# Kernel tuning notes

Hardware: AMD Instinct MI355X
Metric: run time of the kernel (lower is better)

Reference implementation:

```python
import jax, jax.numpy as jnp
import numpy as np

B, N, C, H, P, DP = 2, 1024, 768, 12, 4, 64
CH = C // H
SCALE = CH ** -0.5
EPS = 1e-5


def setup_inputs() -> dict:
    key = jax.random.key(0)
    ks = jax.random.split(key, 24)
    w = lambda k, s: jax.random.normal(k, s, jnp.float32) * 0.02
    inp = {
        'single': jax.random.normal(ks[0], (B, N, C), jnp.float32),
        'pair': jax.random.normal(ks[1], (B, N, N, DP), jnp.float32),
        'rot': jax.random.normal(ks[2], (B, N, 3, 3), jnp.float32),
        'trans': jax.random.normal(ks[3], (B, N, 3), jnp.float32),
        'mask': jnp.ones((B, N), dtype=bool),
        'Wq': w(ks[4], (C, C)), 'bq': jnp.zeros((C,), jnp.float32),
        'Wk': w(ks[5], (C, C)), 'bk': jnp.zeros((C,), jnp.float32),
        'Wv': w(ks[6], (C, C)), 'bv': jnp.zeros((C,), jnp.float32),
        'Wpb': w(ks[7], (DP, H)), 'bpb': jnp.zeros((H,), jnp.float32),
        'Wqp': w(ks[8], (C, H * P * 3)), 'bqp': jnp.zeros((H * P * 3,), jnp.float32),
        'Wkp': w(ks[9], (C, H * P * 3)), 'bkp': jnp.zeros((H * P * 3,), jnp.float32),
        'Wvp': w(ks[10], (C, H * P * 3)), 'bvp': jnp.zeros((H * P * 3,), jnp.float32),
        'Wo': w(ks[11], (C, C)), 'bo': jnp.zeros((C,), jnp.float32),
        'Wpo': w(ks[12], (H * P * 3, C)), 'bpo': jnp.zeros((C,), jnp.float32),
        'gamma': jnp.ones((C,), jnp.float32), 'beta': jnp.zeros((C,), jnp.float32),
    }
    return inp


def _ipa(single, pair, rot, trans, mask,
         Wq, bq, Wk, bk, Wv, bv, Wpb, bpb,
         Wqp, bqp, Wkp, bkp, Wvp, bvp,
         Wo, bo, Wpo, bpo, gamma, beta):
    # scalar q/k/v: [B,N,H,CH]
    q = (single @ Wq + bq).reshape(B, N, H, CH)
    k = (single @ Wk + bk).reshape(B, N, H, CH)
    v = (single @ Wv + bv).reshape(B, N, H, CH)
    # pair bias: [B,H,N,N]
    pair_bias = jnp.transpose(pair @ Wpb + bpb, (0, 3, 1, 2))
    # point q/k/v in local frames: [B,N,H,P,3]
    q_pts = (single @ Wqp + bqp).reshape(B, N, H, P, 3)
    k_pts = (single @ Wkp + bkp).reshape(B, N, H, P, 3)
    v_pts = (single @ Wvp + bvp).reshape(B, N, H, P, 3)
    # rotate into global frame and translate
    t = trans[:, :, None, None, :]  # [B,N,1,1,3]
    rt = lambda pts: jnp.einsum('bnhpd,bnde->bnhpe', pts, rot) + t
    q_pts, k_pts, v_pts = rt(q_pts), rt(k_pts), rt(v_pts)
    # squared norms: [B,H,N]
    q2 = jnp.transpose((q_pts ** 2).sum((3, 4)), (0, 2, 1))
    k2 = jnp.transpose((k_pts ** 2).sum((3, 4)), (0, 2, 1))
    # logits [B,H,M,N]
    scalar_logits = jnp.einsum('bmhc,bnhc->bhmn', q, k) * SCALE
    qk_pts = jnp.einsum('bmhpd,bnhpd->bhmn', q_pts, k_pts)
    point_logits = -0.5 * (q2[:, :, :, None] + k2[:, :, None, :] - 2.0 * qk_pts) * SCALE
    logits = scalar_logits + point_logits + pair_bias
    mask2d = mask[:, None, :, None] & mask[:, None, None, :]
    logits = jnp.where(mask2d, logits, -1e9)
    attn = jax.nn.softmax(logits, axis=-1)
    # dual output aggregation
    out_scalar = jnp.einsum('bhmn,bnhc->bmhc', attn, v).reshape(B, N, C)
    out_points = jnp.einsum('bhmn,bnhpd->bmhpd', attn, v_pts).reshape(B, N, H * P * 3)
    out = (out_scalar @ Wo + bo) + (out_points @ Wpo + bpo)
    x = single + out
    mu = x.mean(-1, keepdims=True)
    var = ((x - mu) ** 2).mean(-1, keepdims=True)
    return (x - mu) * jax.lax.rsqrt(var + EPS) * gamma + beta


def reference(single, pair, rot, trans, mask,
              Wq, bq, Wk, bk, Wv, bv, Wpb, bpb,
              Wqp, bqp, Wkp, bkp, Wvp, bvp,
              Wo, bo, Wpo, bpo, gamma, beta):
    return _ipa(single, pair, rot, trans, mask,
                Wq, bq, Wk, bk, Wv, bv, Wpb, bpb,
                Wqp, bqp, Wkp, bkp, Wvp, bvp,
                Wo, bo, Wpo, bpo, gamma, beta)
```

## Files before the change

kernel.cpp:

```cpp
#include <hip/hip_runtime.h>
#include <hip/hip_bf16.h>

#define B_ 2
#define N_ 1024
#define C_ 768
#define H_ 12
#define CH_ 64
#define P_ 4
#define DP_ 64
#define HP3 144
#define SCALE_ 0.125f
#define FATS 2816
#define K2_ 960
#define NCHUNK 2

typedef __attribute__((ext_vector_type(8))) short short8;
typedef __attribute__((ext_vector_type(4))) float f32x4;

__device__ __forceinline__ short f2bf(float f) {
  __hip_bfloat16 h = __float2bfloat16(f);
  return *reinterpret_cast<short*>(&h);
}
__device__ __forceinline__ float bf2f(unsigned short u) {
  __hip_bfloat16 h;
  *reinterpret_cast<unsigned short*>(&h) = u;
  return __bfloat162float(h);
}

__global__ __launch_bounds__(256) void prep_misc(
    const float* __restrict__ single, unsigned short* __restrict__ Sbf,
    const float* __restrict__ Wq, const float* __restrict__ Wk,
    const float* __restrict__ Wv, const float* __restrict__ Wqp,
    const float* __restrict__ Wkp, const float* __restrict__ Wvp,
    unsigned short* __restrict__ WT1,
    const float* __restrict__ Wo, const float* __restrict__ Wpo,
    unsigned short* __restrict__ W2T,
    const float* __restrict__ bq, const float* __restrict__ bk,
    const float* __restrict__ bv, const float* __restrict__ bqp,
    const float* __restrict__ bkp, const float* __restrict__ bvp,
    const float* __restrict__ bo, const float* __restrict__ bpo,
    float* __restrict__ bcat1, float* __restrict__ bias2)
{
  __shared__ float t[16][17];
  const int tid = threadIdx.x;
  const int bid = blockIdx.x;
  if (bid < 8448) {
    const int bx = bid % 48, by = bid / 48;
    const int rr = tid >> 4, cc = tid & 15;
    const int kk0 = bx * 16, nn0 = by * 16;
    const float* W = nullptr; int ncol0 = 0, Nw = 768;
    if (nn0 < 2304) {
      int s = nn0 / 768;
      W = (s == 0) ? Wq : (s == 1 ? Wk : Wv);
      ncol0 = nn0 - s * 768; Nw = 768;
    } else if (nn0 < 2736) {
      int s = (nn0 - 2304) / 144;
      W = (s == 0) ? Wqp : (s == 1 ? Wkp : Wvp);
      ncol0 = nn0 - 2304 - s * 144; Nw = 144;
    }
    t[rr][cc] = W ? W[(size_t)(kk0 + rr) * Nw + ncol0 + cc] : 0.f;
    __syncthreads();
    WT1[(size_t)(nn0 + rr) * 768 + kk0 + cc] = (unsigned short)f2bf(t[cc][rr]);
  } else if (bid < 11328) {
    const int lb = bid - 8448;
    const int bx = lb % 60, by = lb / 60;
    const int rr = tid >> 4, cc = tid & 15;
    const int kk0 = bx * 16, nn0 = by * 16;
    const int k2 = kk0 + rr, h = k2 / 80, c80 = k2 - h * 80;
    float v = 0.f;
    if (c80 < 64)      v = Wo[(size_t)(h * 64 + c80) * 768 + nn0 + cc];
    else if (c80 < 76) v = Wpo[(size_t)(h * 12 + c80 - 64) * 768 + nn0 + cc];
    t[rr][cc] = v;
    __syncthreads();
    W2T[(size_t)(nn0 + rr) * 960 + kk0 + cc] = (unsigned short)f2bf(t[cc][rr]);
  } else if (bid < 11339) {
    const int idx = (bid - 11328) * 256 + tid;
    if (idx < 2816) {
      float v = 0.f;
      if (idx < 2304) { int s = idx / 768; const float* p = s == 0 ? bq : (s == 1 ? bk : bv); v = p[idx - s * 768]; }
      else if (idx < 2736) { int s = (idx - 2304) / 144; const float* p = s == 0 ? bqp : (s == 1 ? bkp : bvp); v = p[idx - 2304 - s * 144]; }
      bcat1[idx] = v;
    }
    if (idx < 768) bias2[idx] = bo[idx] + bpo[idx];
  } else {
    const int idx = (bid - 11339) * 256 + tid;
    const float4 v = reinterpret_cast<const float4*>(single)[idx];
    union { unsigned short u[4]; uint2 v2; } o;
    o.u[0] = (unsigned short)f2bf(v.x); o.u[1] = (unsigned short)f2bf(v.y);
    o.u[2] = (unsigned short)f2bf(v.z); o.u[3] = (unsigned short)f2bf(v.w);
    reinterpret_cast<uint2*>(Sbf)[idx] = o.v2;
  }
}

template<int BM>
__global__ __launch_bounds__(256) void gemm_bf16(
    const unsigned short* __restrict__ A, int lda,
    const unsigned short* __restrict__ BT, int ldb, int K,
    float* __restrict__ out, int ldo, const float* __restrict__ bias)
{
  constexpr int BN = 64;
  constexpr int MI = BM / 32;
  constexpr int NJ = 2;
  __shared__ __align__(16) unsigned short As[BM][40];
  __shared__ __align__(16) unsigned short Bs[BN][40];
  const int tid = threadIdx.x;
  const int w = tid >> 6, l = tid & 63, r16 = l & 15, g = l >> 4;
  const int wr = w >> 1, wc = w & 1;
  const int bm = blockIdx.y * BM, bn = blockIdx.x * BN;
  f32x4 acc[MI][NJ];
  #pragma unroll
  for (int mi = 0; mi < MI; ++mi)
    #pragma unroll
    for (int nj = 0; nj < NJ; ++nj) {
      acc[mi][nj][0] = 0.f; acc[mi][nj][1] = 0.f;
      acc[mi][nj][2] = 0.f; acc[mi][nj][3] = 0.f;
    }
  for (int k0 = 0; k0 < K; k0 += 32) {
    #pragma unroll
    for (int i = 0; i < BM / 64; ++i) {
      const int idx = tid + 256 * i;
      const int row = idx >> 2, q4 = idx & 3;
      *(uint4*)&As[row][q4 * 8] =
          *(const uint4*)&A[(size_t)(bm + row) * lda + k0 + q4 * 8];
    }
    {
      const int row = tid >> 2, q4 = tid & 3;
      if (row < BN)
        *(uint4*)&Bs[row][q4 * 8] =
            *(const uint4*)&BT[(size_t)(bn + row) * ldb + k0 + q4 * 8];
    }
    __syncthreads();
    short8 af[MI], bfr[NJ];
    #pragma unroll
    for (int mi = 0; mi < MI; ++mi)
      af[mi] = *(const short8*)&As[wr * (BM / 2) + mi * 16 + r16][g * 8];
    #pragma unroll
    for (int nj = 0; nj < NJ; ++nj)
      bfr[nj] = *(const short8*)&Bs[wc * 32 + nj * 16 + r16][g * 8];
    #pragma unroll
    for (int mi = 0; mi < MI; ++mi)
      #pragma unroll
      for (int nj = 0; nj < NJ; ++nj)
        acc[mi][nj] = __builtin_amdgcn_mfma_f32_16x16x32_bf16(
            af[mi], bfr[nj], acc[mi][nj], 0, 0, 0);
    __syncthreads();
  }
  #pragma unroll
  for (int mi = 0; mi < MI; ++mi)
    #pragma unroll
    for (int nj = 0; nj < NJ; ++nj) {
      const int n = bn + wc * 32 + nj * 16 + r16;
      const float bn_ = bias[n];
      #pragma unroll
      for (int reg = 0; reg < 4; ++reg) {
        const int m = bm + wr * (BM / 2) + mi * 16 + g * 4 + reg;
        out[(size_t)m * ldo + n] = acc[mi][nj][reg] + bn_;
      }
    }
}

__global__ __launch_bounds__(128) void prep_qkv(
    const float* __restrict__ fat, const float* __restrict__ rot,
    const float* __restrict__ trans,
    __hip_bfloat16* __restrict__ Qaug, __hip_bfloat16* __restrict__ Kaug,
    __hip_bfloat16* __restrict__ Vtg)
{
  __shared__ float pts[3][12];
  __shared__ float s2[2];
  const int tid = threadIdx.x;
  const int bn = blockIdx.x, h = blockIdx.y;
  const int b = bn >> 10, n = bn & 1023;
  const int bh = b * H_ + h;
  const float* row = fat + (size_t)bn * FATS;
  if (tid < 36) {
    const int set = tid / 12, j = tid - set * 12;
    const int p = j / 3, e = j - p * 3;
    const float* src = row + 2304 + set * 144 + h * 12 + p * 3;
    const float d0 = src[0], d1 = src[1], d2 = src[2];
    const float* rr = rot + (size_t)bn * 9;
    pts[set][j] = d0 * rr[e] + d1 * rr[3 + e] + d2 * rr[6 + e]
                  + trans[(size_t)bn * 3 + e];
  }
  __syncthreads();
  if (tid < 2) {
    float s = 0.f;
    #pragma unroll
    for (int j = 0; j < 12; ++j) s += pts[tid][j] * pts[tid][j];
    s2[tid] = s;
  }
  __syncthreads();
  const int c = tid;
  if (c < 96) {
    float qv, kv;
    if (c < 64) {
      qv = SCALE_ * row[h * CH_ + c];
      kv = row[768 + h * CH_ + c];
    } else if (c < 76) {
      qv = SCALE_ * pts[0][c - 64];
      kv = pts[1][c - 64];
    } else if (c == 76) {
      qv = -0.5f * SCALE_ * s2[0];
      kv = 1.0f;
    } else if (c == 77) {
      qv = -0.5f * SCALE_;
      kv = s2[1];
    } else { qv = 0.f; kv = 0.f; }
    const size_t orow = ((size_t)bh << 10) + n;
    Qaug[orow * 96 + c] = __float2bfloat16(qv);
    Kaug[orow * 96 + c] = __float2bfloat16(kv);
  }
  if (c < 80) {
    float vv = 0.f;
    if (c < 64) vv = row[1536 + h * CH_ + c];
    else if (c < 76) vv = pts[2][c - 64];
    Vtg[(((size_t)bh * 80 + c) << 10) + n] = __float2bfloat16(vv);
  }
}

__global__ __launch_bounds__(256) void pair_bias_mfma(
    const float* __restrict__ pair, const float* __restrict__ Wpb,
    const float* __restrict__ bpb, unsigned short* __restrict__ pb)
{
  __shared__ __align__(16) short WpbT[16][72];
  __shared__ float bpb_s[16];
  __shared__ unsigned short PBs[256][18];
  const int tid = threadIdx.x;
  const int w = tid >> 6, l = tid & 63, r16 = l & 15, g = l >> 4;
  const size_t F0 = (size_t)blockIdx.x * 256;
  const int b = (int)(F0 >> 20);
  const int mn0 = (int)(F0 & 1048575);
  #pragma unroll
  for (int i = 0; i < 4; ++i) {
    int idx = tid + 256 * i;
    int hh = idx & 15, d = idx >> 4;
    WpbT[hh][d] = f2bf(hh < 12 ? Wpb[d * 12 + hh] : 0.f);
  }
  if (tid < 16) bpb_s[tid] = (tid < 12) ? bpb[tid] : 0.f;
  __syncthreads();
  const float4* p4 = (const float4*)pair;
  #pragma unroll
  for (int rg = 0; rg < 4; ++rg) {
    const size_t Fr = F0 + w * 64 + rg * 16 + r16;
    const float bias = bpb_s[r16];
    f32x4 acc;
    acc[0] = bias; acc[1] = bias; acc[2] = bias; acc[3] = bias;
    #pragma unroll
    for (int ks = 0; ks < 2; ++ks) {
      const float4 a0 = p4[Fr * 16 + g * 2 + ks * 8];
      const float4 a1 = p4[Fr * 16 + g * 2 + ks * 8 + 1];
      short8 ap;
      ap[0] = f2bf(a0.x); ap[1] = f2bf(a0.y); ap[2] = f2bf(a0.z); ap[3] = f2bf(a0.w);
      ap[4] = f2bf(a1.x); ap[5] = f2bf(a1.y); ap[6] = f2bf(a1.z); ap[7] = f2bf(a1.w);
      const short8 bw = *(const short8*)&WpbT[r16][ks * 32 + g * 8];
      acc = __builtin_amdgcn_mfma_f32_16x16x32_bf16(ap, bw, acc, 0, 0, 0);
    }
    #pragma unroll
    for (int reg = 0; reg < 4; ++reg)
      PBs[w * 64 + rg * 16 + 4 * g + reg][r16] = (unsigned short)f2bf(acc[reg]);
  }
  __syncthreads();
  #pragma unroll
  for (int hh = 0; hh < 12; ++hh)
    pb[((size_t)(b * 12 + hh) << 20) + mn0 + tid] = PBs[tid][hh];
}

__global__ __launch_bounds__(256) void flash_attn_part(
    const __hip_bfloat16* __restrict__ Qaug, const __hip_bfloat16* __restrict__ Kaug,
    const __hip_bfloat16* __restrict__ Vtg, const unsigned short* __restrict__ pb,
    float* __restrict__ pacc, float* __restrict__ pml)
{
  __shared__ __align__(16) short Ks[64][104];
  __shared__ __align__(16) short Vt[80][72];
  __shared__ __align__(16) short Ps[64][72];
  const int tid = threadIdx.x;
  const int w = tid >> 6, l = tid & 63, r16 = l & 15, g = l >> 4;
  const int m0 = blockIdx.x * 64;
  const int h = blockIdx.y;
  const int b = blockIdx.z >> 1, chunk = blockIdx.z & 1;
  const int bh = b * H_ + h;
  const uint4* Kg = (const uint4*)Kaug;
  const uint4* Vg = (const uint4*)Vtg;
  short8 qreg[3];
  {
    const unsigned short* qrow =
        (const unsigned short*)Qaug + (size_t)((bh << 10) + m0 + w * 16 + r16) * 96;
    #pragma unroll
    for (int ks = 0; ks < 3; ++ks)
      qreg[ks] = *(const short8*)&qrow[ks * 32 + g * 8];
  }
  float rm[4], rl[4];
  f32x4 acc[5];
  #pragma unroll
  for (int r = 0; r < 4; ++r) { rm[r] = -1e30f; rl[r] = 0.f; }
  #pragma unroll
  for (int ct = 0; ct < 5; ++ct) {
    acc[ct][0] = 0.f; acc[ct][1] = 0.f; acc[ct][2] = 0.f; acc[ct][3] = 0.f;
  }
  for (int t = chunk * (16 / NCHUNK); t < (chunk + 1) * (16 / NCHUNK); ++t) {
    const int n0 = t * 64;
    {
      const int r = tid >> 2, q = tid & 3;
      #pragma unroll
      for (int i = 0; i < 3; ++i) {
        const int c8 = q + 4 * i;
        *(uint4*)&Ks[r][c8 * 8] = Kg[(size_t)((bh << 10) + n0 + r) * 12 + c8];
      }
      #pragma unroll
      for (int i = 0; i < 3; ++i) {
        const int ch = tid + 256 * i;
        if (ch < 640) {
          const int cc = ch >> 3, j8 = ch & 7;
          *(uint4*)&Vt[cc][j8 * 8] = Vg[(size_t)(bh * 80 + cc) * 128 + (n0 >> 3) + j8];
        }
      }
    }
    f32x4 s[4];
    {
      const unsigned short* pbrow = pb + ((size_t)bh << 20) + n0 + r16;
      #pragma unroll
      for (int j = 0; j < 4; ++j)
        #pragma unroll
        for (int reg = 0; reg < 4; ++reg)
          s[j][reg] = bf2f(pbrow[((size_t)(m0 + w * 16 + 4 * g + reg) << 10) + 16 * j]);
    }
    __syncthreads();
    #pragma unroll
    for (int ks = 0; ks < 3; ++ks) {
      #pragma unroll
      for (int j = 0; j < 4; ++j) {
        const short8 bK = *(const short8*)&Ks[16 * j + r16][ks * 32 + g * 8];
        s[j] = __builtin_amdgcn_mfma_f32_16x16x32_bf16(qreg[ks], bK, s[j], 0, 0, 0);
      }
    }
    #pragma unroll
    for (int reg = 0; reg < 4; ++reg) {
      float tm = fmaxf(fmaxf(s[0][reg], s[1][reg]), fmaxf(s[2][reg], s[3][reg]));
      tm = fmaxf(tm, __shfl_xor(tm, 1));
      tm = fmaxf(tm, __shfl_xor(tm, 2));
      tm = fmaxf(tm, __shfl_xor(tm, 4));
      tm = fmaxf(tm, __shfl_xor(tm, 8));
      const float nm = fmaxf(rm[reg], tm);
      const float fac = __expf(rm[reg] - nm);
      rm[reg] = nm;
      float ps = 0.f;
      #pragma unroll
      for (int j = 0; j < 4; ++j) {
        const float p = __expf(s[j][reg] - nm);
        s[j][reg] = p;
        ps += p;
      }
      ps += __shfl_xor(ps, 1);
      ps += __shfl_xor(ps, 2);
      ps += __shfl_xor(ps, 4);
      ps += __shfl_xor(ps, 8);
      rl[reg] = rl[reg] * fac + ps;
      #pragma unroll
      for (int ct = 0; ct < 5; ++ct) acc[ct][reg] *= fac;
    }
    #pragma unroll
    for (int j = 0; j < 4; ++j)
      #pragma unroll
      for (int reg = 0; reg < 4; ++reg)
        Ps[w * 16 + 4 * g + reg][16 * j + r16] = f2bf(s[j][reg]);
    __syncthreads();
    #pragma unroll
    for (int ks = 0; ks < 2; ++ks) {
      const short8 aP = *(const short8*)&Ps[w * 16 + r16][ks * 32 + g * 8];
      #pragma unroll
      for (int ct = 0; ct < 5; ++ct) {
        const short8 bV = *(const short8*)&Vt[ct * 16 + r16][ks * 32 + g * 8];
        acc[ct] = __builtin_amdgcn_mfma_f32_16x16x32_bf16(aP, bV, acc[ct], 0, 0, 0);
      }
    }
    __syncthreads();
  }
  #pragma unroll
  for (int reg = 0; reg < 4; ++reg) {
    const int row = (bh << 10) + m0 + w * 16 + 4 * g + reg;
    const size_t base = ((size_t)chunk * 24576 + row) * 80;
    #pragma unroll
    for (int ct = 0; ct < 5; ++ct)
      pacc[base + ct * 16 + r16] = acc[ct][reg];
    if (r16 == 0) {
      pml[((size_t)chunk * 24576 + row) * 2]     = rm[reg];
      pml[((size_t)chunk * 24576 + row) * 2 + 1] = rl[reg];
    }
  }
}

__global__ __launch_bounds__(256) void flash_combine(
    const float* __restrict__ pacc, const float* __restrict__ pml,
    unsigned short* __restrict__ fused)
{
  const int tid = threadIdx.x;
  const int r = tid >> 4, cg = tid & 15;
  const int row = blockIdx.x * 16 + r;
  const int bh = row >> 10, m = row & 1023;
  const int b = bh / 12, h = bh - b * 12;
  const float m0 = pml[(size_t)row * 2], l0 = pml[(size_t)row * 2 + 1];
  const float m1 = pml[((size_t)24576 + row) * 2], l1 = pml[((size_t)24576 + row) * 2 + 1];
  const float M = fmaxf(m0, m1);
  const float w0 = __expf(m0 - M), w1 = __expf(m1 - M);
  const float inv = 1.f / (l0 * w0 + l1 * w1);
  const size_t mg = (size_t)(b * N_ + m);
  #pragma unroll
  for (int i = 0; i < 5; ++i) {
    const int c = cg * 5 + i;
    const float a0 = pacc[(size_t)row * 80 + c];
    const float a1 = pacc[((size_t)24576 + row) * 80 + c];
    fused[mg * K2_ + h * 80 + c] = (unsigned short)f2bf((a0 * w0 + a1 * w1) * inv);
  }
}

__global__ __launch_bounds__(256) void ln_kernel(
    const float* __restrict__ single, const float* __restrict__ tmp,
    const float* __restrict__ gamma, const float* __restrict__ beta,
    float* __restrict__ out)
{
  __shared__ float x_s[C_];
  __shared__ float rs1[4], rs2[4];
  const int row = blockIdx.x, tid = threadIdx.x;
  const int lane = tid & 63, wave = tid >> 6;
  const size_t base = (size_t)row * C_;
  float s1 = 0.f, s2 = 0.f;
  for (int i = tid; i < C_; i += 256) {
    float x = single[base + i] + tmp[base + i];
    x_s[i] = x;
    s1 += x;
    s2 += x * x;
  }
  #pragma unroll
  for (int off = 32; off > 0; off >>= 1) {
    s1 += __shfl_xor(s1, off);
    s2 += __shfl_xor(s2, off);
  }
  if (!lane) { rs1[wave] = s1; rs2[wave] = s2; }
  __syncthreads();
  const float S1 = rs1[0] + rs1[1] + rs1[2] + rs1[3];
  const float S2 = rs2[0] + rs2[1] + rs2[2] + rs2[3];
  const float mu = S1 * (1.f / C_);
  const float var = S2 * (1.f / C_) - mu * mu;
  const float inv = rsqrtf(var + 1e-5f);
  for (int i = tid; i < C_; i += 256)
    out[base + i] = (x_s[i] - mu) * inv * gamma[i] + beta[i];
}

extern "C" void kernel_launch(void* const* d_in, const int* in_sizes, int n_in,
                              void* d_out, int out_size, void* d_ws, size_t ws_size,
                              hipStream_t stream) {
  const float* single = (const float*)d_in[0];
  const float* pair   = (const float*)d_in[1];
  const float* rot    = (const float*)d_in[2];
  const float* trans  = (const float*)d_in[3];
  const float* Wq  = (const float*)d_in[5];
  const float* bq  = (const float*)d_in[6];
  const float* Wk  = (const float*)d_in[7];
  const float* bk  = (const float*)d_in[8];
  const float* Wv  = (const float*)d_in[9];
  const float* bv  = (const float*)d_in[10];
  const float* Wpb = (const float*)d_in[11];
  const float* bpb = (const float*)d_in[12];
  const float* Wqp = (const float*)d_in[13];
  const float* bqp = (const float*)d_in[14];
  const float* Wkp = (const float*)d_in[15];
  const float* bkp = (const float*)d_in[16];
  const float* Wvp = (const float*)d_in[17];
  const float* bvp = (const float*)d_in[18];
  const float* Wo  = (const float*)d_in[19];
  const float* bo  = (const float*)d_in[20];
  const float* Wpo = (const float*)d_in[21];
  const float* bpo = (const float*)d_in[22];
  const float* gamma = (const float*)d_in[23];
  const float* beta  = (const float*)d_in[24];

  float* ws = (float*)d_ws;
  float* fat  = ws;
  float* tmpb = ws + 5767168;
  unsigned short* pbb  = (unsigned short*)(ws + 7340032);
  __hip_bfloat16* Qaug = (__hip_bfloat16*)(ws + 19922944);
  __hip_bfloat16* Kaug = (__hip_bfloat16*)(ws + 21102592);
  __hip_bfloat16* Vtg  = (__hip_bfloat16*)(ws + 22282240);
  unsigned short* Sbf  = (unsigned short*)(ws + 23265280);
  unsigned short* WT1  = (unsigned short*)(ws + 24051712);
  unsigned short* W2T  = (unsigned short*)(ws + 25133056);
  float* bcat1 = ws + 25501696;
  float* bias2 = ws + 25504512;
  unsigned short* fusedb = (unsigned short*)(ws + 25505536);
  float* pacc = ws + 26488576;
  float* pml  = ws + 30420736;

  const dim3 blk(256);
  prep_misc<<<12875, blk, 0, stream>>>(single, Sbf, Wq, Wk, Wv, Wqp, Wkp, Wvp,
                                       WT1, Wo, Wpo, W2T, bq, bk, bv, bqp, bkp,
                                       bvp, bo, bpo, bcat1, bias2);
  gemm_bf16<128><<<dim3(44, 16), blk, 0, stream>>>(Sbf, 768, WT1, 768, 768,
                                                   fat, FATS, bcat1);
  prep_qkv<<<dim3(2048, 12), dim3(128), 0, stream>>>(fat, rot, trans, Qaug, Kaug, Vtg);
  pair_bias_mfma<<<8192, blk, 0, stream>>>(pair, Wpb, bpb, pbb);
  flash_attn_part<<<dim3(16, 12, 2 * NCHUNK), blk, 0, stream>>>(
      Qaug, Kaug, Vtg, pbb, pacc, pml);
  flash_combine<<<1536, blk, 0, stream>>>(pacc, pml, fusedb);
  gemm_bf16<64><<<dim3(12, 32), blk, 0, stream>>>(fusedb, K2_, W2T, K2_, K2_,
                                                  tmpb, 768, bias2);
  ln_kernel<<<2048, blk, 0, stream>>>(single, tmpb, gamma, beta, (float*)d_out);
}
```

Measured before the change: 249.3 us.

## Fuse pair-bias projection into flash attention with 8-way key split

Merges the pair-bias MFMA kernel into the attention kernel, so each block computes the bias tile for all 12 heads in shared memory and consumes it immediately. This removes the bf16 pair-bias round trip through global memory. The key dimension is split into 8 chunks, K and V are read directly from global rather than staged in LDS, and the partial accumulators are stored in bf16. The trade-offs are a larger combine step, extra rounding of the partials, and higher register pressure from three heads per wave.

```diff
diff --git a/kernel.cpp b/kernel.cpp
--- a/kernel.cpp
+++ b/kernel.cpp
@@ -12,7 +12,7 @@
 #define SCALE_ 0.125f
 #define FATS 2816
 #define K2_ 960
-#define NCHUNK 2
+#define NCH 8
 
 typedef __attribute__((ext_vector_type(8))) short short8;
 typedef __attribute__((ext_vector_type(4))) float f32x4;
@@ -217,179 +217,171 @@
   }
 }
 
-__global__ __launch_bounds__(256) void pair_bias_mfma(
+__global__ __launch_bounds__(256) void ipa_fused(
     const float* __restrict__ pair, const float* __restrict__ Wpb,
-    const float* __restrict__ bpb, unsigned short* __restrict__ pb)
+    const float* __restrict__ bpb,
+    const __hip_bfloat16* __restrict__ Qaug,
+    const __hip_bfloat16* __restrict__ Kaug,
+    const __hip_bfloat16* __restrict__ Vtg,
+    unsigned short* __restrict__ pacc, float* __restrict__ pml)
 {
   __shared__ __align__(16) short WpbT[16][72];
   __shared__ float bpb_s[16];
-  __shared__ unsigned short PBs[256][18];
+  __shared__ unsigned short pb_s[12 * 1058];
+  __shared__ __align__(16) unsigned short Ps[4 * 1056];
   const int tid = threadIdx.x;
   const int w = tid >> 6, l = tid & 63, r16 = l & 15, g = l >> 4;
-  const size_t F0 = (size_t)blockIdx.x * 256;
-  const int b = (int)(F0 >> 20);
-  const int mn0 = (int)(F0 & 1048575);
-  #pragma unroll
-  for (int i = 0; i < 4; ++i) {
-    int idx = tid + 256 * i;
-    int hh = idx & 15, d = idx >> 4;
+  const int bid = blockIdx.x;
+  const int combo = bid & 15, mtile = bid >> 4;
+  const int b = combo >> 3, chunk = combo & 7;
+  const int m0 = mtile * 16;
+
+  for (int i = tid; i < 1024; i += 256) {
+    const int hh = i & 15, d = i >> 4;
     WpbT[hh][d] = f2bf(hh < 12 ? Wpb[d * 12 + hh] : 0.f);
   }
   if (tid < 16) bpb_s[tid] = (tid < 12) ? bpb[tid] : 0.f;
+
+  short8 qf[3][3];
+  #pragma unroll
+  for (int hh = 0; hh < 3; ++hh) {
+    const int bh = b * H_ + w * 3 + hh;
+    const unsigned short* qrow = (const unsigned short*)Qaug
+        + (size_t)((bh << 10) + m0 + r16) * 96;
+    #pragma unroll
+    for (int ks = 0; ks < 3; ++ks)
+      qf[hh][ks] = *(const short8*)&qrow[ks * 32 + g * 8];
+  }
+  float rm[3][4], rl[3][4];
+  f32x4 oacc[3][5];
+  #pragma unroll
+  for (int hh = 0; hh < 3; ++hh) {
+    #pragma unroll
+    for (int r = 0; r < 4; ++r) { rm[hh][r] = -1e30f; rl[hh][r] = 0.f; }
+    #pragma unroll
+    for (int ct = 0; ct < 5; ++ct) {
+      oacc[hh][ct][0] = 0.f; oacc[hh][ct][1] = 0.f;
+      oacc[hh][ct][2] = 0.f; oacc[hh][ct][3] = 0.f;
+    }
+  }
   __syncthreads();
-  const float4* p4 = (const float4*)pair;
-  #pragma unroll
-  for (int rg = 0; rg < 4; ++rg) {
-    const size_t Fr = F0 + w * 64 + rg * 16 + r16;
-    const float bias = bpb_s[r16];
-    f32x4 acc;
-    acc[0] = bias; acc[1] = bias; acc[2] = bias; acc[3] = bias;
-    #pragma unroll
-    for (int ks = 0; ks < 2; ++ks) {
-      const float4 a0 = p4[Fr * 16 + g * 2 + ks * 8];
-      const float4 a1 = p4[Fr * 16 + g * 2 + ks * 8 + 1];
-      short8 ap;
-      ap[0] = f2bf(a0.x); ap[1] = f2bf(a0.y); ap[2] = f2bf(a0.z); ap[3] = f2bf(a0.w);
-      ap[4] = f2bf(a1.x); ap[5] = f2bf(a1.y); ap[6] = f2bf(a1.z); ap[7] = f2bf(a1.w);
-      const short8 bw = *(const short8*)&WpbT[r16][ks * 32 + g * 8];
-      acc = __builtin_amdgcn_mfma_f32_16x16x32_bf16(ap, bw, acc, 0, 0, 0);
-    }
-    #pragma unroll
-    for (int reg = 0; reg < 4; ++reg)
-      PBs[w * 64 + rg * 16 + 4 * g + reg][r16] = (unsigned short)f2bf(acc[reg]);
-  }
-  __syncthreads();
-  #pragma unroll
-  for (int hh = 0; hh < 12; ++hh)
-    pb[((size_t)(b * 12 + hh) << 20) + mn0 + tid] = PBs[tid][hh];
-}
-
-__global__ __launch_bounds__(256) void flash_attn_part(
-    const __hip_bfloat16* __restrict__ Qaug, const __hip_bfloat16* __restrict__ Kaug,
-    const __hip_bfloat16* __restrict__ Vtg, const unsigned short* __restrict__ pb,
-    float* __restrict__ pacc, float* __restrict__ pml)
-{
-  __shared__ __align__(16) short Ks[64][104];
-  __shared__ __align__(16) short Vt[80][72];
-  __shared__ __align__(16) short Ps[64][72];
-  const int tid = threadIdx.x;
-  const int w = tid >> 6, l = tid & 63, r16 = l & 15, g = l >> 4;
-  const int m0 = blockIdx.x * 64;
-  const int h = blockIdx.y;
-  const int b = blockIdx.z >> 1, chunk = blockIdx.z & 1;
-  const int bh = b * H_ + h;
-  const uint4* Kg = (const uint4*)Kaug;
-  const uint4* Vg = (const uint4*)Vtg;
-  short8 qreg[3];
-  {
-    const unsigned short* qrow =
-        (const unsigned short*)Qaug + (size_t)((bh << 10) + m0 + w * 16 + r16) * 96;
-    #pragma unroll
-    for (int ks = 0; ks < 3; ++ks)
-      qreg[ks] = *(const short8*)&qrow[ks * 32 + g * 8];
-  }
-  float rm[4], rl[4];
-  f32x4 acc[5];
-  #pragma unroll
-  for (int r = 0; r < 4; ++r) { rm[r] = -1e30f; rl[r] = 0.f; }
-  #pragma unroll
-  for (int ct = 0; ct < 5; ++ct) {
-    acc[ct][0] = 0.f; acc[ct][1] = 0.f; acc[ct][2] = 0.f; acc[ct][3] = 0.f;
-  }
-  for (int t = chunk * (16 / NCHUNK); t < (chunk + 1) * (16 / NCHUNK); ++t) {
-    const int n0 = t * 64;
-    {
-      const int r = tid >> 2, q = tid & 3;
-      #pragma unroll
-      for (int i = 0; i < 3; ++i) {
-        const int c8 = q + 4 * i;
-        *(uint4*)&Ks[r][c8 * 8] = Kg[(size_t)((bh << 10) + n0 + r) * 12 + c8];
-      }
-      #pragma unroll
-      for (int i = 0; i < 3; ++i) {
-        const int ch = tid + 256 * i;
-        if (ch < 640) {
-          const int cc = ch >> 3, j8 = ch & 7;
-          *(uint4*)&Vt[cc][j8 * 8] = Vg[(size_t)(bh * 80 + cc) * 128 + (n0 >> 3) + j8];
+
+  for (int t = 0; t < 2; ++t) {
+    const int n0 = chunk * 128 + t * 64;
+    #pragma unroll 4
+    for (int sub = 0; sub < 16; ++sub) {
+      const int fr = w * 256 + sub * 16 + r16;
+      const int ml = fr >> 6, nn = fr & 63;
+      const float* src = pair
+          + ((((size_t)(b << 10) + m0 + ml) << 10) + n0 + nn) * 64;
+      f32x4 a;
+      a[0] = bpb_s[r16]; a[1] = a[0]; a[2] = a[0]; a[3] = a[0];
+      #pragma unroll
+      for (int ks = 0; ks < 2; ++ks) {
+        const f32x4 a0 = __builtin_nontemporal_load(
+            reinterpret_cast<const f32x4*>(src + ks * 32 + g * 8));
+        const f32x4 a1 = __builtin_nontemporal_load(
+            reinterpret_cast<const f32x4*>(src + ks * 32 + g * 8 + 4));
+        short8 ap;
+        ap[0] = f2bf(a0[0]); ap[1] = f2bf(a0[1]); ap[2] = f2bf(a0[2]); ap[3] = f2bf(a0[3]);
+        ap[4] = f2bf(a1[0]); ap[5] = f2bf(a1[1]); ap[6] = f2bf(a1[2]); ap[7] = f2bf(a1[3]);
+        const short8 bw = *(const short8*)&WpbT[r16][ks * 32 + g * 8];
+        a = __builtin_amdgcn_mfma_f32_16x16x32_bf16(ap, bw, a, 0, 0, 0);
+      }
+      if (r16 < 12) {
+        #pragma unroll
+        for (int reg = 0; reg < 4; ++reg) {
+          const int fr2 = w * 256 + sub * 16 + 4 * g + reg;
+          pb_s[r16 * 1058 + (fr2 >> 6) * 66 + (fr2 & 63)] =
+              (unsigned short)f2bf(a[reg]);
         }
       }
     }
-    f32x4 s[4];
-    {
-      const unsigned short* pbrow = pb + ((size_t)bh << 20) + n0 + r16;
+    __syncthreads();
+    #pragma unroll
+    for (int hh = 0; hh < 3; ++hh) {
+      const int h = w * 3 + hh;
+      const int bh = b * H_ + h;
+      f32x4 s[4];
       #pragma unroll
       for (int j = 0; j < 4; ++j)
         #pragma unroll
         for (int reg = 0; reg < 4; ++reg)
-          s[j][reg] = bf2f(pbrow[((size_t)(m0 + w * 16 + 4 * g + reg) << 10) + 16 * j]);
+          s[j][reg] = bf2f(pb_s[h * 1058 + (4 * g + reg) * 66 + 16 * j + r16]);
+      #pragma unroll
+      for (int ks = 0; ks < 3; ++ks) {
+        #pragma unroll
+        for (int j = 0; j < 4; ++j) {
+          const unsigned short* kr = (const unsigned short*)Kaug
+              + (size_t)((bh << 10) + n0 + 16 * j + r16) * 96 + ks * 32 + g * 8;
+          s[j] = __builtin_amdgcn_mfma_f32_16x16x32_bf16(
+              qf[hh][ks], *(const short8*)kr, s[j], 0, 0, 0);
+        }
+      }
+      #pragma unroll
+      for (int reg = 0; reg < 4; ++reg) {
+        float tm = fmaxf(fmaxf(s[0][reg], s[1][reg]), fmaxf(s[2][reg], s[3][reg]));
+        tm = fmaxf(tm, __shfl_xor(tm, 1));
+        tm = fmaxf(tm, __shfl_xor(tm, 2));
+        tm = fmaxf(tm, __shfl_xor(tm, 4));
+        tm = fmaxf(tm, __shfl_xor(tm, 8));
+        const float nm = fmaxf(rm[hh][reg], tm);
+        const float fac = __expf(rm[hh][reg] - nm);
+        rm[hh][reg] = nm;
+        float ps = 0.f;
+        #pragma unroll
+        for (int j = 0; j < 4; ++j) {
+          const float p = __expf(s[j][reg] - nm);
+          s[j][reg] = p;
+          ps += p;
+        }
+        ps += __shfl_xor(ps, 1);
+        ps += __shfl_xor(ps, 2);
+        ps += __shfl_xor(ps, 4);
+        ps += __shfl_xor(ps, 8);
+        rl[hh][reg] = rl[hh][reg] * fac + ps;
+        #pragma unroll
+        for (int ct = 0; ct < 5; ++ct) oacc[hh][ct][reg] *= fac;
+      }
+      #pragma unroll
+      for (int j = 0; j < 4; ++j)
+        #pragma unroll
+        for (int reg = 0; reg < 4; ++reg)
+          Ps[w * 1056 + (4 * g + reg) * 66 + 16 * j + r16] = (unsigned short)f2bf(s[j][reg]);
+      #pragma unroll
+      for (int ks = 0; ks < 2; ++ks) {
+        const short8 aP = *(const short8*)&Ps[w * 1056 + r16 * 66 + ks * 32 + g * 8];
+        #pragma unroll
+        for (int ct = 0; ct < 5; ++ct) {
+          const unsigned short* vr = (const unsigned short*)Vtg
+              + (((size_t)(bh * 80 + ct * 16 + r16)) << 10) + n0 + ks * 32 + g * 8;
+          oacc[hh][ct] = __builtin_amdgcn_mfma_f32_16x16x32_bf16(
+              aP, *(const short8*)vr, oacc[hh][ct], 0, 0, 0);
+        }
+      }
     }
     __syncthreads();
-    #pragma unroll
-    for (int ks = 0; ks < 3; ++ks) {
-      #pragma unroll
-      for (int j = 0; j < 4; ++j) {
-        const short8 bK = *(const short8*)&Ks[16 * j + r16][ks * 32 + g * 8];
-        s[j] = __builtin_amdgcn_mfma_f32_16x16x32_bf16(qreg[ks], bK, s[j], 0, 0, 0);
-      }
-    }
+  }
+  #pragma unroll
+  for (int hh = 0; hh < 3; ++hh) {
+    const int bh = b * H_ + w * 3 + hh;
     #pragma unroll
     for (int reg = 0; reg < 4; ++reg) {
-      float tm = fmaxf(fmaxf(s[0][reg], s[1][reg]), fmaxf(s[2][reg], s[3][reg]));
-      tm = fmaxf(tm, __shfl_xor(tm, 1));
-      tm = fmaxf(tm, __shfl_xor(tm, 2));
-      tm = fmaxf(tm, __shfl_xor(tm, 4));
-      tm = fmaxf(tm, __shfl_xor(tm, 8));
-      const float nm = fmaxf(rm[reg], tm);
-      const float fac = __expf(rm[reg] - nm);
-      rm[reg] = nm;
-      float ps = 0.f;
-      #pragma unroll
-      for (int j = 0; j < 4; ++j) {
-        const float p = __expf(s[j][reg] - nm);
-        s[j][reg] = p;
-        ps += p;
-      }
-      ps += __shfl_xor(ps, 1);
-      ps += __shfl_xor(ps, 2);
-      ps += __shfl_xor(ps, 4);
-      ps += __shfl_xor(ps, 8);
-      rl[reg] = rl[reg] * fac + ps;
-      #pragma unroll
-      for (int ct = 0; ct < 5; ++ct) acc[ct][reg] *= fac;
-    }
-    #pragma unroll
-    for (int j = 0; j < 4; ++j)
-      #pragma unroll
-      for (int reg = 0; reg < 4; ++reg)
-        Ps[w * 16 + 4 * g + reg][16 * j + r16] = f2bf(s[j][reg]);
-    __syncthreads();
-    #pragma unroll
-    for (int ks = 0; ks < 2; ++ks) {
-      const short8 aP = *(const short8*)&Ps[w * 16 + r16][ks * 32 + g * 8];
-      #pragma unroll
-      for (int ct = 0; ct < 5; ++ct) {
-        const short8 bV = *(const short8*)&Vt[ct * 16 + r16][ks * 32 + g * 8];
-        acc[ct] = __builtin_amdgcn_mfma_f32_16x16x32_bf16(aP, bV, acc[ct], 0, 0, 0);
-      }
-    }
-    __syncthreads();
-  }
-  #pragma unroll
-  for (int reg = 0; reg < 4; ++reg) {
-    const int row = (bh << 10) + m0 + w * 16 + 4 * g + reg;
-    const size_t base = ((size_t)chunk * 24576 + row) * 80;
-    #pragma unroll
-    for (int ct = 0; ct < 5; ++ct)
-      pacc[base + ct * 16 + r16] = acc[ct][reg];
-    if (r16 == 0) {
-      pml[((size_t)chunk * 24576 + row) * 2]     = rm[reg];
-      pml[((size_t)chunk * 24576 + row) * 2 + 1] = rl[reg];
+      const int row = (bh << 10) + m0 + 4 * g + reg;
+      const size_t base = ((size_t)chunk * 24576 + row) * 80;
+      #pragma unroll
+      for (int ct = 0; ct < 5; ++ct)
+        pacc[base + ct * 16 + r16] = (unsigned short)f2bf(oacc[hh][ct][reg]);
+      if (r16 == 0) {
+        pml[((size_t)chunk * 24576 + row) * 2]     = rm[hh][reg];
+        pml[((size_t)chunk * 24576 + row) * 2 + 1] = rl[hh][reg];
+      }
     }
   }
 }
 
 __global__ __launch_bounds__(256) void flash_combine(
-    const float* __restrict__ pacc, const float* __restrict__ pml,
+    const unsigned short* __restrict__ pacc, const float* __restrict__ pml,
     unsigned short* __restrict__ fused)
 {
   const int tid = threadIdx.x;
@@ -397,18 +389,31 @@
   const int row = blockIdx.x * 16 + r;
   const int bh = row >> 10, m = row & 1023;
   const int b = bh / 12, h = bh - b * 12;
-  const float m0 = pml[(size_t)row * 2], l0 = pml[(size_t)row * 2 + 1];
-  const float m1 = pml[((size_t)24576 + row) * 2], l1 = pml[((size_t)24576 + row) * 2 + 1];
-  const float M = fmaxf(m0, m1);
-  const float w0 = __expf(m0 - M), w1 = __expf(m1 - M);
-  const float inv = 1.f / (l0 * w0 + l1 * w1);
+  float mv[NCH], lv[NCH];
+  float M = -1e30f;
+  #pragma unroll
+  for (int ch = 0; ch < NCH; ++ch) {
+    mv[ch] = pml[((size_t)ch * 24576 + row) * 2];
+    lv[ch] = pml[((size_t)ch * 24576 + row) * 2 + 1];
+    M = fmaxf(M, mv[ch]);
+  }
+  float den = 0.f;
+  float wch[NCH];
+  #pragma unroll
+  for (int ch = 0; ch < NCH; ++ch) {
+    wch[ch] = __expf(mv[ch] - M);
+    den += lv[ch] * wch[ch];
+  }
+  const float inv = 1.f / den;
   const size_t mg = (size_t)(b * N_ + m);
   #pragma unroll
   for (int i = 0; i < 5; ++i) {
     const int c = cg * 5 + i;
-    const float a0 = pacc[(size_t)row * 80 + c];
-    const float a1 = pacc[((size_t)24576 + row) * 80 + c];
-    fused[mg * K2_ + h * 80 + c] = (unsigned short)f2bf((a0 * w0 + a1 * w1) * inv);
+    float a = 0.f;
+    #pragma unroll
+    for (int ch = 0; ch < NCH; ++ch)
+      a += bf2f(pacc[((size_t)ch * 24576 + row) * 80 + c]) * wch[ch];
+    fused[mg * K2_ + h * 80 + c] = (unsigned short)f2bf(a * inv);
   }
 }
 
@@ -476,18 +481,17 @@
   float* ws = (float*)d_ws;
   float* fat  = ws;
   float* tmpb = ws + 5767168;
-  unsigned short* pbb  = (unsigned short*)(ws + 7340032);
-  __hip_bfloat16* Qaug = (__hip_bfloat16*)(ws + 19922944);
-  __hip_bfloat16* Kaug = (__hip_bfloat16*)(ws + 21102592);
-  __hip_bfloat16* Vtg  = (__hip_bfloat16*)(ws + 22282240);
-  unsigned short* Sbf  = (unsigned short*)(ws + 23265280);
-  unsigned short* WT1  = (unsigned short*)(ws + 24051712);
-  unsigned short* W2T  = (unsigned short*)(ws + 25133056);
-  float* bcat1 = ws + 25501696;
-  float* bias2 = ws + 25504512;
-  unsigned short* fusedb = (unsigned short*)(ws + 25505536);
-  float* pacc = ws + 26488576;
-  float* pml  = ws + 30420736;
+  __hip_bfloat16* Qaug = (__hip_bfloat16*)(ws + 7340032);
+  __hip_bfloat16* Kaug = (__hip_bfloat16*)(ws + 8519680);
+  __hip_bfloat16* Vtg  = (__hip_bfloat16*)(ws + 9699328);
+  unsigned short* Sbf  = (unsigned short*)(ws + 10682368);
+  unsigned short* WT1  = (unsigned short*)(ws + 11468800);
+  unsigned short* W2T  = (unsigned short*)(ws + 12550144);
+  float* bcat1 = ws + 12918784;
+  float* bias2 = ws + 12921600;
+  unsigned short* fusedb = (unsigned short*)(ws + 12922368);
+  unsigned short* pacc = (unsigned short*)(ws + 13905408);
+  float* pml  = ws + 21769728;
 
   const dim3 blk(256);
   prep_misc<<<12875, blk, 0, stream>>>(single, Sbf, Wq, Wk, Wv, Wqp, Wkp, Wvp,
@@ -496,9 +500,7 @@
   gemm_bf16<128><<<dim3(44, 16), blk, 0, stream>>>(Sbf, 768, WT1, 768, 768,
                                                    fat, FATS, bcat1);
   prep_qkv<<<dim3(2048, 12), dim3(128), 0, stream>>>(fat, rot, trans, Qaug, Kaug, Vtg);
-  pair_bias_mfma<<<8192, blk, 0, stream>>>(pair, Wpb, bpb, pbb);
-  flash_attn_part<<<dim3(16, 12, 2 * NCHUNK), blk, 0, stream>>>(
-      Qaug, Kaug, Vtg, pbb, pacc, pml);
+  ipa_fused<<<1024, blk, 0, stream>>>(pair, Wpb, bpb, Qaug, Kaug, Vtg, pacc, pml);
   flash_combine<<<1536, blk, 0, stream>>>(pacc, pml, fusedb);
   gemm_bf16<64><<<dim3(12, 32), blk, 0, stream>>>(fusedb, K2_, W2T, K2_, K2_,
                                                   tmpb, 768, bias2);
```

Measured after the change: 281.3 us. 1.13x slower.

## Fuse split-KV combine into output GEMM, store partials in bf16, nontemporal pair loads

Applied to the files above, without the earlier changes.

Removes the flash_combine kernel by doing the two-chunk softmax merge inside a new GEMM kernel's A-tile load, computing per-row/head weights from pml in shared memory. The attention partial accumulators are now stored as bf16 instead of fp32, halving that traffic. Pair-bias loads use nontemporal loads to avoid polluting cache with the large pair tensor. Costs: extra rounding of partials to bf16, and a simple 64x64 GEMM with no double buffering that may be slower than the prior gemm_bf16.

```diff
diff --git a/kernel.cpp b/kernel.cpp
--- a/kernel.cpp
+++ b/kernel.cpp
@@ -237,20 +237,22 @@
   }
   if (tid < 16) bpb_s[tid] = (tid < 12) ? bpb[tid] : 0.f;
   __syncthreads();
-  const float4* p4 = (const float4*)pair;
   #pragma unroll
   for (int rg = 0; rg < 4; ++rg) {
     const size_t Fr = F0 + w * 64 + rg * 16 + r16;
+    const float* src = pair + Fr * 64;
     const float bias = bpb_s[r16];
     f32x4 acc;
     acc[0] = bias; acc[1] = bias; acc[2] = bias; acc[3] = bias;
     #pragma unroll
     for (int ks = 0; ks < 2; ++ks) {
-      const float4 a0 = p4[Fr * 16 + g * 2 + ks * 8];
-      const float4 a1 = p4[Fr * 16 + g * 2 + ks * 8 + 1];
+      const f32x4 a0 = __builtin_nontemporal_load(
+          reinterpret_cast<const f32x4*>(src + ks * 32 + g * 8));
+      const f32x4 a1 = __builtin_nontemporal_load(
+          reinterpret_cast<const f32x4*>(src + ks * 32 + g * 8 + 4));
       short8 ap;
-      ap[0] = f2bf(a0.x); ap[1] = f2bf(a0.y); ap[2] = f2bf(a0.z); ap[3] = f2bf(a0.w);
-      ap[4] = f2bf(a1.x); ap[5] = f2bf(a1.y); ap[6] = f2bf(a1.z); ap[7] = f2bf(a1.w);
+      ap[0] = f2bf(a0[0]); ap[1] = f2bf(a0[1]); ap[2] = f2bf(a0[2]); ap[3] = f2bf(a0[3]);
+      ap[4] = f2bf(a1[0]); ap[5] = f2bf(a1[1]); ap[6] = f2bf(a1[2]); ap[7] = f2bf(a1[3]);
       const short8 bw = *(const short8*)&WpbT[r16][ks * 32 + g * 8];
       acc = __builtin_amdgcn_mfma_f32_16x16x32_bf16(ap, bw, acc, 0, 0, 0);
     }
@@ -267,7 +269,7 @@
 __global__ __launch_bounds__(256) void flash_attn_part(
     const __hip_bfloat16* __restrict__ Qaug, const __hip_bfloat16* __restrict__ Kaug,
     const __hip_bfloat16* __restrict__ Vtg, const unsigned short* __restrict__ pb,
-    float* __restrict__ pacc, float* __restrict__ pml)
+    unsigned short* __restrict__ pacc, float* __restrict__ pml)
 {
   __shared__ __align__(16) short Ks[64][104];
   __shared__ __align__(16) short Vt[80][72];
@@ -380,7 +382,7 @@
     const size_t base = ((size_t)chunk * 24576 + row) * 80;
     #pragma unroll
     for (int ct = 0; ct < 5; ++ct)
-      pacc[base + ct * 16 + r16] = acc[ct][reg];
+      pacc[base + ct * 16 + r16] = (unsigned short)f2bf(acc[ct][reg]);
     if (r16 == 0) {
       pml[((size_t)chunk * 24576 + row) * 2]     = rm[reg];
       pml[((size_t)chunk * 24576 + row) * 2 + 1] = rl[reg];
@@ -388,28 +390,88 @@
   }
 }
 
-__global__ __launch_bounds__(256) void flash_combine(
-    const float* __restrict__ pacc, const float* __restrict__ pml,
-    unsigned short* __restrict__ fused)
-{
+__global__ __launch_bounds__(256) void gemm2_fused(
+    const unsigned short* __restrict__ pacc, const float* __restrict__ pml,
+    const unsigned short* __restrict__ BT, float* __restrict__ out,
+    const float* __restrict__ bias)
+{
+  __shared__ __align__(16) unsigned short As[64][40];
+  __shared__ __align__(16) unsigned short Bs[64][40];
+  __shared__ float w0_s[64][12], w1_s[64][12];
   const int tid = threadIdx.x;
-  const int r = tid >> 4, cg = tid & 15;
-  const int row = blockIdx.x * 16 + r;
-  const int bh = row >> 10, m = row & 1023;
-  const int b = bh / 12, h = bh - b * 12;
-  const float m0 = pml[(size_t)row * 2], l0 = pml[(size_t)row * 2 + 1];
-  const float m1 = pml[((size_t)24576 + row) * 2], l1 = pml[((size_t)24576 + row) * 2 + 1];
-  const float M = fmaxf(m0, m1);
-  const float w0 = __expf(m0 - M), w1 = __expf(m1 - M);
-  const float inv = 1.f / (l0 * w0 + l1 * w1);
-  const size_t mg = (size_t)(b * N_ + m);
-  #pragma unroll
-  for (int i = 0; i < 5; ++i) {
-    const int c = cg * 5 + i;
-    const float a0 = pacc[(size_t)row * 80 + c];
-    const float a1 = pacc[((size_t)24576 + row) * 80 + c];
-    fused[mg * K2_ + h * 80 + c] = (unsigned short)f2bf((a0 * w0 + a1 * w1) * inv);
-  }
+  const int w = tid >> 6, l = tid & 63, r16 = l & 15, g = l >> 4;
+  const int wr = w >> 1, wc = w & 1;
+  const int bm = blockIdx.y * 64, bn = blockIdx.x * 64;
+  for (int i = tid; i < 64 * 12; i += 256) {
+    const int row = i / 12, h = i - row * 12;
+    const int grow = bm + row;
+    const int b = grow >> 10, m = grow & 1023;
+    const size_t pr = ((size_t)(b * 12 + h) << 10) + m;
+    const float m0 = pml[pr * 2],              l0 = pml[pr * 2 + 1];
+    const float m1 = pml[(24576 + pr) * 2],    l1 = pml[(24576 + pr) * 2 + 1];
+    const float M = fmaxf(m0, m1);
+    const float e0 = __expf(m0 - M), e1 = __expf(m1 - M);
+    const float inv = 1.f / (l0 * e0 + l1 * e1);
+    w0_s[row][h] = e0 * inv;
+    w1_s[row][h] = e1 * inv;
+  }
+  f32x4 acc[2][2];
+  #pragma unroll
+  for (int mi = 0; mi < 2; ++mi)
+    #pragma unroll
+    for (int nj = 0; nj < 2; ++nj) {
+      acc[mi][nj][0] = 0.f; acc[mi][nj][1] = 0.f;
+      acc[mi][nj][2] = 0.f; acc[mi][nj][3] = 0.f;
+    }
+  __syncthreads();
+  for (int k0 = 0; k0 < 960; k0 += 32) {
+    {
+      const int row = tid >> 2, q4 = tid & 3;
+      const int k2 = k0 + q4 * 8;
+      const int h = k2 / 80, c = k2 - h * 80;
+      const int grow = bm + row;
+      const int b = grow >> 10, m = grow & 1023;
+      const size_t pr = ((size_t)(b * 12 + h) << 10) + m;
+      const short8 p0 = *(const short8*)&pacc[pr * 80 + c];
+      const short8 p1 = *(const short8*)&pacc[(size_t)24576 * 80 + pr * 80 + c];
+      const float w0 = w0_s[row][h], w1 = w1_s[row][h];
+      short8 av;
+      #pragma unroll
+      for (int j = 0; j < 8; ++j)
+        av[j] = f2bf(bf2f((unsigned short)p0[j]) * w0 +
+                     bf2f((unsigned short)p1[j]) * w1);
+      *(short8*)&As[row][q4 * 8] = av;
+      *(uint4*)&Bs[row][q4 * 8] =
+          *(const uint4*)&BT[(size_t)(bn + row) * 960 + k0 + q4 * 8];
+    }
+    __syncthreads();
+    short8 af[2], bfr[2];
+    #pragma unroll
+    for (int mi = 0; mi < 2; ++mi)
+      af[mi] = *(const short8*)&As[wr * 32 + mi * 16 + r16][g * 8];
+    #pragma unroll
+    for (int nj = 0; nj < 2; ++nj)
+      bfr[nj] = *(const short8*)&Bs[wc * 32 + nj * 16 + r16][g * 8];
+    #pragma unroll
+    for (int mi = 0; mi < 2; ++mi)
+      #pragma unroll
+      for (int nj = 0; nj < 2; ++nj)
+        acc[mi][nj] = __builtin_amdgcn_mfma_f32_16x16x32_bf16(
+            af[mi], bfr[nj], acc[mi][nj], 0, 0, 0);
+    __syncthreads();
+  }
+  #pragma unroll
+  for (int mi = 0; mi < 2; ++mi)
+    #pragma unroll
+    for (int nj = 0; nj < 2; ++nj) {
+      const int n = bn + wc * 32 + nj * 16 + r16;
+      const float bn_ = bias[n];
+      #pragma unroll
+      for (int reg = 0; reg < 4; ++reg) {
+        const int m = bm + wr * 32 + mi * 16 + g * 4 + reg;
+        out[(size_t)m * 768 + n] = acc[mi][nj][reg] + bn_;
+      }
+    }
 }
 
 __global__ __launch_bounds__(256) void ln_kernel(
@@ -485,8 +547,7 @@
   unsigned short* W2T  = (unsigned short*)(ws + 25133056);
   float* bcat1 = ws + 25501696;
   float* bias2 = ws + 25504512;
-  unsigned short* fusedb = (unsigned short*)(ws + 25505536);
-  float* pacc = ws + 26488576;
+  unsigned short* pacc = (unsigned short*)(ws + 26488576);
   float* pml  = ws + 30420736;
 
   const dim3 blk(256);
@@ -499,8 +560,6 @@
   pair_bias_mfma<<<8192, blk, 0, stream>>>(pair, Wpb, bpb, pbb);
   flash_attn_part<<<dim3(16, 12, 2 * NCHUNK), blk, 0, stream>>>(
       Qaug, Kaug, Vtg, pbb, pacc, pml);
-  flash_combine<<<1536, blk, 0, stream>>>(pacc, pml, fusedb);
-  gemm_bf16<64><<<dim3(12, 32), blk, 0, stream>>>(fusedb, K2_, W2T, K2_, K2_,
-                                                  tmpb, 768, bias2);
+  gemm2_fused<<<dim3(12, 32), blk, 0, stream>>>(pacc, pml, W2T, tmpb, bias2);
   ln_kernel<<<2048, blk, 0, stream>>>(single, tmpb, gamma, beta, (float*)d_out);
 }
```

New measurement: 251.3 us. Within noise of the previous version (+0.8%).
